# Kernel optimization log

Hardware: AMD Instinct MI355X
Metric: run time of the kernel (lower is better)

Reference implementation:

```python
import jax, jax.numpy as jnp
import numpy as np

EPS = 1e-5
B, N, K = 2, 20000, 17      # batch, num points, k+1 neighbors
CIN = 128                   # bn_size * growth_rate
G = 128                     # growth_rate


def index_points(pts, idx):
    # pts: [B, C, N], idx: [B, S, K] -> [B, C, S, K]
    return jnp.take_along_axis(pts[:, :, :, None], idx[:, None, :, :], axis=2)


def conv_bn_relu(x, W, b, gamma, beta, mean, var):
    # 1x1 Conv2d + BatchNorm2d (inference, running stats) + ReLU
    # x: [B, Cin, N, K], W: [Cout, Cin]
    y = jnp.einsum('oc,bcnk->bonk', W, x) + b[None, :, None, None]
    inv = gamma / jnp.sqrt(var + EPS)
    y = y * inv[None, :, None, None] + (beta - mean * inv)[None, :, None, None]
    return jax.nn.relu(y)


def setup_inputs() -> dict:
    key = jax.random.key(0)
    ks = jax.random.split(key, 16)
    feats = jax.random.normal(ks[0], (B, CIN, N), dtype=jnp.float32)
    pts = jax.random.normal(ks[1], (B, 3, N), dtype=jnp.float32)
    knn_idx = jax.random.randint(ks[2], (B, N, K), 0, N, dtype=jnp.int32)
    s = 0.05
    d = {
        'feats': feats, 'pts': pts, 'knn_idx': knn_idx,
        'Wd': jax.random.normal(ks[3], (G, 3), dtype=jnp.float32) * s,
        'bd': jnp.zeros((G,), jnp.float32),
        'gd': jnp.ones((G,), jnp.float32),
        'betad': jnp.zeros((G,), jnp.float32),
        'md': jax.random.normal(ks[4], (G,), dtype=jnp.float32) * 0.01,
        'vd': jax.random.uniform(ks[5], (G,), jnp.float32, 0.5, 1.5),
        'Wf': jax.random.normal(ks[6], (G, CIN), dtype=jnp.float32) * s,
        'bf': jnp.zeros((G,), jnp.float32),
        'gf': jnp.ones((G,), jnp.float32),
        'betaf': jnp.zeros((G,), jnp.float32),
        'mf': jax.random.normal(ks[7], (G,), dtype=jnp.float32) * 0.01,
        'vf': jax.random.uniform(ks[8], (G,), jnp.float32, 0.5, 1.5),
        'Wp': jax.random.normal(ks[9], (G, G), dtype=jnp.float32) * s,
        'bp': jnp.zeros((G,), jnp.float32),
        'gp': jnp.ones((G,), jnp.float32),
        'betap': jnp.zeros((G,), jnp.float32),
        'mp': jax.random.normal(ks[10], (G,), dtype=jnp.float32) * 0.01,
        'vp': jax.random.uniform(ks[11], (G,), jnp.float32, 0.5, 1.5),
    }
    return d


def reference(feats, pts, knn_idx,
              Wd, bd, gd, betad, md, vd,
              Wf, bf, gf, betaf, mf, vf,
              Wp, bp, gp, betap, mp, vp):
    # Point3DConv.forward with precomputed knn_idx
    knn_pts = index_points(pts, knn_idx)                 # [B,3,N,K]
    knn_delta = knn_pts - pts[:, :, :, None]             # [B,3,N,K]
    knn_delta = conv_bn_relu(knn_delta, Wd, bd, gd, betad, md, vd)   # [B,G,N,K]
    knn_feats = index_points(feats, knn_idx)              # [B,CIN,N,K]
    knn_feats = conv_bn_relu(knn_feats, Wf, bf, gf, betaf, mf, vf)   # [B,G,N,K]
    new_feats = knn_delta * knn_feats                     # [B,G,N,K]
    new_feats = conv_bn_relu(new_feats, Wp, bp, gp, betap, mp, vp)   # [B,G,N,K]
    return new_feats.sum(axis=-1)                         # [B,G,N]
```

## Files before the change

kernel.cpp:

```cpp
#include <hip/hip_runtime.h>
#include <hip/hip_bf16.h>
#include <cstdint>
#include <cstddef>

#define NB 2
#define NPT 20000
#define KNN 17
#define CH 128
#define NT16 (NPT/16)
#define NT32 (NPT/32)
#define EPSV 1e-5f

typedef short short8 __attribute__((ext_vector_type(8)));
typedef float f32x4 __attribute__((ext_vector_type(4)));
typedef float f32x2 __attribute__((ext_vector_type(2)));
typedef unsigned short u16;

__device__ __forceinline__ unsigned cvtpk(float lo, float hi) {
    unsigned r;
    asm("v_cvt_pk_bf16_f32 %0, %1, %2" : "=v"(r) : "v"(lo), "v"(hi));
    return r;
}
__device__ __forceinline__ u16 f2bf1(float x) {
    return (u16)cvtpk(x, x);
}
__device__ __forceinline__ f32x2 bfpair(unsigned w) {
    union { unsigned u; float f; } lo, hi;
    lo.u = w << 16; hi.u = w & 0xffff0000u;
    f32x2 r; r[0] = lo.f; r[1] = hi.f; return r;
}
__device__ __forceinline__ short8 packrow_scaled(const float* wrow, float s) {
    float4 w0 = *(const float4*)(wrow);
    float4 w1 = *(const float4*)(wrow + 4);
    uint4 uu;
    uu.x = cvtpk(w0.x*s, w0.y*s); uu.y = cvtpk(w0.z*s, w0.w*s);
    uu.z = cvtpk(w1.x*s, w1.y*s); uu.w = cvtpk(w1.z*s, w1.w*s);
    union { uint4 u; short8 s8; } cv; cv.u = uu; return cv.s8;
}
__device__ __forceinline__ short8 packrow(const float* wrow) {
    return packrow_scaled(wrow, 1.0f);
}
__device__ __forceinline__ void lds_barrier() {
    asm volatile("s_waitcnt lgkmcnt(0)\n\ts_barrier" ::: "memory");
}

__global__ __launch_bounds__(256) void k_feats(
    const float* __restrict__ feats, const float* __restrict__ Wf,
    const float* __restrict__ bfv, const float* __restrict__ gf,
    const float* __restrict__ betaf, const float* __restrict__ mf,
    const float* __restrict__ vf, u16* __restrict__ Fout)
{
    __shared__ u16 A_lds[32][136];
    __shared__ u16 O_lds[32][136];
    const int t  = threadIdx.x;
    const int b  = blockIdx.x / NT32;
    const int n0 = (blockIdx.x % NT32) * 32;

    {
        const int chunk = t & 7;
        const int cbase = t >> 3;
        const float* base = feats + (size_t)b*CH*NPT + n0 + chunk*4;
        #pragma unroll
        for (int it = 0; it < 4; ++it) {
            int c = it*32 + cbase;
            float4 v = *(const float4*)(base + (size_t)c*NPT);
            A_lds[chunk*4+0][c] = f2bf1(v.x);
            A_lds[chunk*4+1][c] = f2bf1(v.y);
            A_lds[chunk*4+2][c] = f2bf1(v.z);
            A_lds[chunk*4+3][c] = f2bf1(v.w);
        }
    }

    const int lane = t & 63, wid = t >> 6;
    const int h = lane >> 4, r16 = lane & 15;
    const int gb = wid * 32;

    short8 bfrag[2][4];
    float sf[2], tf[2];
    #pragma unroll
    for (int T = 0; T < 2; ++T) {
        int g = gb + T*16 + r16;
        #pragma unroll
        for (int s = 0; s < 4; ++s)
            bfrag[T][s] = packrow(Wf + g*CH + s*32 + h*8);
        float inv = gf[g] * rsqrtf(vf[g] + EPSV);
        sf[T] = inv;
        tf[T] = bfv[g]*inv + betaf[g] - mf[g]*inv;
    }
    lds_barrier();

    #pragma unroll
    for (int sub = 0; sub < 2; ++sub) {
        short8 a[4];
        #pragma unroll
        for (int s = 0; s < 4; ++s)
            a[s] = *(const short8*)&A_lds[sub*16 + r16][s*32 + h*8];
        #pragma unroll
        for (int T = 0; T < 2; ++T) {
            f32x4 acc = {0.f, 0.f, 0.f, 0.f};
            #pragma unroll
            for (int s = 0; s < 4; ++s)
                acc = __builtin_amdgcn_mfma_f32_16x16x32_bf16(a[s], bfrag[T][s], acc, 0, 0, 0);
            #pragma unroll
            for (int r = 0; r < 4; ++r) {
                float y = fmaxf(fmaf(sf[T], acc[r], tf[T]), 0.f);
                O_lds[sub*16 + 4*h + r][gb + T*16 + r16] = f2bf1(y);
            }
        }
    }
    lds_barrier();

    {
        const int pp = t >> 3, cc = (t & 7) * 16;
        uint4 v0 = *(const uint4*)&O_lds[pp][cc];
        uint4 v1 = *(const uint4*)&O_lds[pp][cc + 8];
        u16* dst = Fout + ((size_t)b*NPT + n0 + pp)*CH + cc;
        *(uint4*)dst = v0;
        *(uint4*)(dst + 8) = v1;
    }
}

struct Pref { float4 m; uint4 f; };

__global__ __launch_bounds__(256) void k_main(
    const float* __restrict__ pts, const int* __restrict__ knn,
    const u16* __restrict__ F,
    const float* __restrict__ Wd, const float* __restrict__ bd,
    const float* __restrict__ gd, const float* __restrict__ betad,
    const float* __restrict__ md, const float* __restrict__ vd,
    const float* __restrict__ Wp, const float* __restrict__ bp,
    const float* __restrict__ gp, const float* __restrict__ betap,
    const float* __restrict__ mp, const float* __restrict__ vp,
    float* __restrict__ out)
{
    __shared__ u16   Abuf[2][16*128];
    __shared__ float4 meta[16][KNN];

    const int t  = threadIdx.x;
    const int b  = blockIdx.x / NT16;
    const int n0 = (blockIdx.x % NT16) * 16;

    const float* px = pts + (size_t)b*3*NPT;
    const float* py = px + NPT;
    const float* pz = py + NPT;

    {
        const int* krow = knn + ((size_t)b*NPT + n0)*KNN;
        #pragma unroll 1
        for (int tau = t; tau < 16*KNN; tau += 256) {
            int r  = tau / KNN;
            int nb = krow[tau];
            float4 m;
            m.x = px[nb] - px[n0+r];
            m.y = py[nb] - py[n0+r];
            m.z = pz[nb] - pz[n0+r];
            m.w = __int_as_float(nb);
            (&meta[0][0])[tau] = m;
        }
    }
    lds_barrier();

    const int p_t = t >> 4, j_t = t & 15, c0 = j_t*8;
    const int lane = t & 63, wid = t >> 6;
    const int h = lane >> 4, r16 = lane & 15;
    const int gb = wid * 32;
    const u16* Fbj = F + (size_t)b*NPT*CH + c0;

    const int wOff = p_t*128 + (c0 ^ ((p_t&7)*8));
    int rOff[4];
    #pragma unroll
    for (int s = 0; s < 4; ++s)
        rOff[s] = r16*128 + ((s*32 + h*8) ^ ((r16&7)*8));

    auto issueK = [&](int k)->Pref {
        Pref P;
        P.m = meta[p_t][k];
        int nb = __float_as_int(P.m.w);
        P.f = *(const uint4*)(Fbj + (size_t)nb*CH);
        return P;
    };

    Pref PA = issueK(0);
    Pref PB = issueK(1);

    short8 bfrag[2][4];
    float tpv[2];
    #pragma unroll
    for (int T = 0; T < 2; ++T) {
        int g = gb + T*16 + r16;
        float inv = gp[g] * rsqrtf(vp[g] + EPSV);
        #pragma unroll
        for (int s = 0; s < 4; ++s)
            bfrag[T][s] = packrow_scaled(Wp + g*CH + s*32 + h*8, inv);
        tpv[T] = bp[g]*inv + betap[g] - mp[g]*inv;
    }

    f32x2 wx2[4], wy2[4], wz2[4], t2[4];
    #pragma unroll
    for (int q = 0; q < 4; ++q) {
        const int ca = c0 + 2*q, cb = ca + 1;
        float inva = gd[ca] * rsqrtf(vd[ca] + EPSV);
        float invb = gd[cb] * rsqrtf(vd[cb] + EPSV);
        wx2[q][0] = Wd[ca*3+0]*inva; wx2[q][1] = Wd[cb*3+0]*invb;
        wy2[q][0] = Wd[ca*3+1]*inva; wy2[q][1] = Wd[cb*3+1]*invb;
        wz2[q][0] = Wd[ca*3+2]*inva; wz2[q][1] = Wd[cb*3+2]*invb;
        t2[q][0]  = bd[ca]*inva + betad[ca] - md[ca]*inva;
        t2[q][1]  = bd[cb]*invb + betad[cb] - md[cb]*invb;
    }

    auto stage = [&](u16* A, const Pref& P) {
        const unsigned fw[4] = {P.f.x, P.f.y, P.f.z, P.f.w};
        const f32x2 z2 = {0.f, 0.f};
        unsigned pk[4];
        #pragma unroll
        for (int q = 0; q < 4; ++q) {
            f32x2 d = wx2[q]*P.m.x + wy2[q]*P.m.y + wz2[q]*P.m.z + t2[q];
            d = __builtin_elementwise_max(d, z2);
            f32x2 pr = d * bfpair(fw[q]);
            pk[q] = cvtpk(pr[0], pr[1]);
        }
        uint4 v; v.x = pk[0]; v.y = pk[1]; v.z = pk[2]; v.w = pk[3];
        *(uint4*)(A + wOff) = v;
    };

    f32x4 facc[2] = {};
    auto mfmaP = [&](const u16* A) {
        short8 a[4];
        #pragma unroll
        for (int s = 0; s < 4; ++s)
            a[s] = *(const short8*)(A + rOff[s]);
        #pragma unroll
        for (int T = 0; T < 2; ++T) {
            f32x4 acc = {0.f,0.f,0.f,0.f};
            #pragma unroll
            for (int s = 0; s < 4; ++s)
                acc = __builtin_amdgcn_mfma_f32_16x16x32_bf16(a[s], bfrag[T][s], acc, 0, 0, 0);
            f32x4 nt = {-tpv[T], -tpv[T], -tpv[T], -tpv[T]};
            facc[T] += __builtin_elementwise_max(acc, nt);
        }
    };

    stage(Abuf[0], PA);
    PA = PB;
    PB = issueK(2);
    lds_barrier();

    int p = 0;
    #pragma unroll 1
    for (int k = 0; k < 16; ++k) {
        stage(Abuf[p^1], PA);
        PA = PB;
        if (k + 3 <= 16) PB = issueK(k+3);
        mfmaP(Abuf[p]);
        lds_barrier();
        p ^= 1;
    }
    mfmaP(Abuf[p]);

    #pragma unroll
    for (int T = 0; T < 2; ++T) {
        int g = gb + T*16 + r16;
        f32x4 o = facc[T] + (float)KNN * tpv[T];
        *(f32x4*)(out + ((size_t)b*CH + g)*NPT + n0 + 4*h) = o;
    }
}

extern "C" void kernel_launch(void* const* d_in, const int* in_sizes, int n_in,
                              void* d_out, int out_size, void* d_ws, size_t ws_size,
                              hipStream_t stream)
{
    const float* feats = (const float*)d_in[0];
    const float* pts   = (const float*)d_in[1];
    const int*   knn   = (const int*)d_in[2];
    const float* Wd    = (const float*)d_in[3];
    const float* bd    = (const float*)d_in[4];
    const float* gd    = (const float*)d_in[5];
    const float* betad = (const float*)d_in[6];
    const float* md    = (const float*)d_in[7];
    const float* vd    = (const float*)d_in[8];
    const float* Wf    = (const float*)d_in[9];
    const float* bfv   = (const float*)d_in[10];
    const float* gf    = (const float*)d_in[11];
    const float* betaf = (const float*)d_in[12];
    const float* mf    = (const float*)d_in[13];
    const float* vf    = (const float*)d_in[14];
    const float* Wp    = (const float*)d_in[15];
    const float* bp    = (const float*)d_in[16];
    const float* gp    = (const float*)d_in[17];
    const float* betap = (const float*)d_in[18];
    const float* mp    = (const float*)d_in[19];
    const float* vp    = (const float*)d_in[20];
    float* out = (float*)d_out;
    u16* Fws = (u16*)d_ws;

    k_feats<<<dim3(NB * NT32), 256, 0, stream>>>(feats, Wf, bfv, gf, betaf, mf, vf, Fws);
    k_main <<<dim3(NB * NT16), 256, 0, stream>>>(pts, knn, Fws, Wd, bd, gd, betad, md, vd,
                                                 Wp, bp, gp, betap, mp, vp, out);
}
```

Measured before the change: 84.01 us.

## Process 32 points per block with 4-plane batched staging and deeper prefetch

The main kernel now handles two 16-point tiles per block, flattening the (tile, neighbor) pairs into 34 planes. Each loop iteration stages and prefetches four planes at a time into double-buffered LDS, which cuts barriers per plane and deepens the gather prefetch. The neighbor index is pre-shifted into a byte offset, and packed fp32 FMA/mul instructions are emitted explicitly. In exchange, the grid has half as many blocks, LDS and register use are larger, and the pipeline tail is hand-unrolled with more complex control.

```diff
diff --git a/kernel.cpp b/kernel.cpp
--- a/kernel.cpp
+++ b/kernel.cpp
@@ -7,8 +7,10 @@
 #define NPT 20000
 #define KNN 17
 #define CH 128
-#define NT16 (NPT/16)
 #define NT32 (NPT/32)
+#define NPB 32
+#define NTILE 2
+#define NPLANES (NTILE*KNN)
 #define EPSV 1e-5f
 
 typedef short short8 __attribute__((ext_vector_type(8)));
@@ -21,8 +23,16 @@
     asm("v_cvt_pk_bf16_f32 %0, %1, %2" : "=v"(r) : "v"(lo), "v"(hi));
     return r;
 }
-__device__ __forceinline__ u16 f2bf1(float x) {
-    return (u16)cvtpk(x, x);
+__device__ __forceinline__ u16 f2bf1(float x) { return (u16)cvtpk(x, x); }
+__device__ __forceinline__ f32x2 pk_fma(f32x2 a, f32x2 b, f32x2 c) {
+    f32x2 d;
+    asm("v_pk_fma_f32 %0, %1, %2, %3" : "=v"(d) : "v"(a), "v"(b), "v"(c));
+    return d;
+}
+__device__ __forceinline__ f32x2 pk_mul(f32x2 a, f32x2 b) {
+    f32x2 d;
+    asm("v_pk_mul_f32 %0, %1, %2" : "=v"(d) : "v"(a), "v"(b));
+    return d;
 }
 __device__ __forceinline__ f32x2 bfpair(unsigned w) {
     union { unsigned u; float f; } lo, hi;
@@ -133,29 +143,32 @@
     const float* __restrict__ mp, const float* __restrict__ vp,
     float* __restrict__ out)
 {
-    __shared__ u16   Abuf[2][16*128];
-    __shared__ float4 meta[16][KNN];
+    __shared__ u16   Abuf[2][4][16*128];
+    __shared__ float4 metaL[NPLANES][16];
 
     const int t  = threadIdx.x;
-    const int b  = blockIdx.x / NT16;
-    const int n0 = (blockIdx.x % NT16) * 16;
+    const int b  = blockIdx.x / NT32;
+    const int n0 = (blockIdx.x % NT32) * NPB;
 
     const float* px = pts + (size_t)b*3*NPT;
     const float* py = px + NPT;
     const float* pz = py + NPT;
 
     {
-        const int* krow = knn + ((size_t)b*NPT + n0)*KNN;
+        const int* kbase = knn + ((size_t)b*NPT + n0)*KNN;
         #pragma unroll 1
-        for (int tau = t; tau < 16*KNN; tau += 256) {
-            int r  = tau / KNN;
-            int nb = krow[tau];
+        for (int e = t; e < NPLANES*16; e += 256) {
+            int pi = e >> 4, p = e & 15;
+            int tile = (pi >= KNN) ? 1 : 0;
+            int k  = pi - tile*KNN;
+            int row = tile*16 + p;
+            int nb = kbase[row*KNN + k];
             float4 m;
-            m.x = px[nb] - px[n0+r];
-            m.y = py[nb] - py[n0+r];
-            m.z = pz[nb] - pz[n0+r];
-            m.w = __int_as_float(nb);
-            (&meta[0][0])[tau] = m;
+            m.x = px[nb] - px[n0+row];
+            m.y = py[nb] - py[n0+row];
+            m.z = pz[nb] - pz[n0+row];
+            m.w = __int_as_float(nb << 8);
+            metaL[pi][p] = m;
         }
     }
     lds_barrier();
@@ -164,7 +177,7 @@
     const int lane = t & 63, wid = t >> 6;
     const int h = lane >> 4, r16 = lane & 15;
     const int gb = wid * 32;
-    const u16* Fbj = F + (size_t)b*NPT*CH + c0;
+    const char* FbjB = (const char*)(F + (size_t)b*NPT*CH + c0);
 
     const int wOff = p_t*128 + (c0 ^ ((p_t&7)*8));
     int rOff[4];
@@ -172,16 +185,16 @@
     for (int s = 0; s < 4; ++s)
         rOff[s] = r16*128 + ((s*32 + h*8) ^ ((r16&7)*8));
 
-    auto issueK = [&](int k)->Pref {
+    auto issueK = [&](int pi)->Pref {
         Pref P;
-        P.m = meta[p_t][k];
-        int nb = __float_as_int(P.m.w);
-        P.f = *(const uint4*)(Fbj + (size_t)nb*CH);
+        P.m = metaL[pi][p_t];
+        P.f = *(const uint4*)(FbjB + __float_as_int(P.m.w));
         return P;
     };
 
-    Pref PA = issueK(0);
-    Pref PB = issueK(1);
+    Pref P[4];
+    #pragma unroll
+    for (int i = 0; i < 4; ++i) P[i] = issueK(i);
 
     short8 bfrag[2][4];
     float tpv[2];
@@ -208,27 +221,28 @@
         t2[q][1]  = bd[cb]*invb + betad[cb] - md[cb]*invb;
     }
 
-    auto stage = [&](u16* A, const Pref& P) {
-        const unsigned fw[4] = {P.f.x, P.f.y, P.f.z, P.f.w};
+    auto stage = [&](u16* plane, const Pref& Pr) {
+        const unsigned fw[4] = {Pr.f.x, Pr.f.y, Pr.f.z, Pr.f.w};
         const f32x2 z2 = {0.f, 0.f};
+        f32x2 dx2 = {Pr.m.x, Pr.m.x}, dy2 = {Pr.m.y, Pr.m.y}, dz2 = {Pr.m.z, Pr.m.z};
         unsigned pk[4];
         #pragma unroll
         for (int q = 0; q < 4; ++q) {
-            f32x2 d = wx2[q]*P.m.x + wy2[q]*P.m.y + wz2[q]*P.m.z + t2[q];
+            f32x2 d = pk_fma(wx2[q], dx2, pk_fma(wy2[q], dy2, pk_fma(wz2[q], dz2, t2[q])));
             d = __builtin_elementwise_max(d, z2);
-            f32x2 pr = d * bfpair(fw[q]);
+            f32x2 pr = pk_mul(d, bfpair(fw[q]));
             pk[q] = cvtpk(pr[0], pr[1]);
         }
         uint4 v; v.x = pk[0]; v.y = pk[1]; v.z = pk[2]; v.w = pk[3];
-        *(uint4*)(A + wOff) = v;
+        *(uint4*)(plane + wOff) = v;
     };
 
     f32x4 facc[2] = {};
-    auto mfmaP = [&](const u16* A) {
+    auto mfmaP = [&](const u16* plane) {
         short8 a[4];
         #pragma unroll
         for (int s = 0; s < 4; ++s)
-            a[s] = *(const short8*)(A + rOff[s]);
+            a[s] = *(const short8*)(plane + rOff[s]);
         #pragma unroll
         for (int T = 0; T < 2; ++T) {
             f32x4 acc = {0.f,0.f,0.f,0.f};
@@ -239,30 +253,57 @@
             facc[T] += __builtin_elementwise_max(acc, nt);
         }
     };
-
-    stage(Abuf[0], PA);
-    PA = PB;
-    PB = issueK(2);
+    auto writeout = [&](int tile) {
+        #pragma unroll
+        for (int T = 0; T < 2; ++T) {
+            int g = gb + T*16 + r16;
+            f32x4 o = facc[T] + (float)KNN * tpv[T];
+            *(f32x4*)(out + ((size_t)b*CH + g)*NPT + n0 + tile*16 + 4*h) = o;
+            facc[T][0]=0.f; facc[T][1]=0.f; facc[T][2]=0.f; facc[T][3]=0.f;
+        }
+    };
+
+    #pragma unroll
+    for (int i = 0; i < 4; ++i) stage(Abuf[0][i], P[i]);
+    #pragma unroll
+    for (int i = 0; i < 4; ++i) P[i] = issueK(4+i);
     lds_barrier();
 
-    int p = 0;
     #pragma unroll 1
-    for (int k = 0; k < 16; ++k) {
-        stage(Abuf[p^1], PA);
-        PA = PB;
-        if (k + 3 <= 16) PB = issueK(k+3);
-        mfmaP(Abuf[p]);
+    for (int c = 0; c < 6; ++c) {
+        const int H = c & 1;
+        u16* sb = &Abuf[H^1][0][0];
+        #pragma unroll
+        for (int i = 0; i < 4; ++i) stage(sb + i*2048, P[i]);
+        #pragma unroll
+        for (int i = 0; i < 4; ++i) P[i] = issueK(4*c + 8 + i);
+        const u16* mb = &Abuf[H][0][0];
+        #pragma unroll
+        for (int i = 0; i < 4; ++i) {
+            mfmaP(mb + i*2048);
+            if (i == 0 && c == 4) writeout(0);
+        }
         lds_barrier();
-        p ^= 1;
-    }
-    mfmaP(Abuf[p]);
-
-    #pragma unroll
-    for (int T = 0; T < 2; ++T) {
-        int g = gb + T*16 + r16;
-        f32x4 o = facc[T] + (float)KNN * tpv[T];
-        *(f32x4*)(out + ((size_t)b*CH + g)*NPT + n0 + 4*h) = o;
-    }
+    }
+    {
+        #pragma unroll
+        for (int i = 0; i < 4; ++i) stage(&Abuf[1][i][0], P[i]);
+        P[0] = issueK(32);
+        P[1] = issueK(33);
+        #pragma unroll
+        for (int i = 0; i < 4; ++i) mfmaP(&Abuf[0][i][0]);
+        lds_barrier();
+    }
+    {
+        stage(&Abuf[0][0][0], P[0]);
+        stage(&Abuf[0][1][0], P[1]);
+        #pragma unroll
+        for (int i = 0; i < 4; ++i) mfmaP(&Abuf[1][i][0]);
+        lds_barrier();
+    }
+    mfmaP(&Abuf[0][0][0]);
+    mfmaP(&Abuf[0][1][0]);
+    writeout(1);
 }
 
 extern "C" void kernel_launch(void* const* d_in, const int* in_sizes, int n_in,
@@ -294,6 +335,6 @@
     u16* Fws = (u16*)d_ws;
 
     k_feats<<<dim3(NB * NT32), 256, 0, stream>>>(feats, Wf, bfv, gf, betaf, mf, vf, Fws);
-    k_main <<<dim3(NB * NT16), 256, 0, stream>>>(pts, knn, Fws, Wd, bd, gd, betad, md, vd,
+    k_main <<<dim3(NB * NT32), 256, 0, stream>>>(pts, knn, Fws, Wd, bd, gd, betad, md, vd,
                                                  Wp, bp, gp, betap, mp, vp, out);
 }
```

New measurement: 75.54 us. 10.1% less time.

## Process neighbor pairs per barrier with deeper prefetch and packed FMA staging

Applied to the files above, without the earlier changes.

Restructures the K-loop so each LDS barrier covers two neighbor slices instead of one. The double buffer now holds two planes per stage, and four neighbor prefetches are kept in flight, which halves the number of barriers and deepens the latency hiding for the gathered feature loads. The meta table is transposed to [K][16], and neighbor indices are pre-shifted to byte offsets so the gather address needs no multiply. The delta conv math is written with explicit v_pk_fma/v_pk_mul. The cost is more registers per thread and a fully hand-unrolled schedule.

```diff
diff --git a/kernel.cpp b/kernel.cpp
--- a/kernel.cpp
+++ b/kernel.cpp
@@ -21,8 +21,16 @@
     asm("v_cvt_pk_bf16_f32 %0, %1, %2" : "=v"(r) : "v"(lo), "v"(hi));
     return r;
 }
-__device__ __forceinline__ u16 f2bf1(float x) {
-    return (u16)cvtpk(x, x);
+__device__ __forceinline__ u16 f2bf1(float x) { return (u16)cvtpk(x, x); }
+__device__ __forceinline__ f32x2 pk_fma(f32x2 a, f32x2 b, f32x2 c) {
+    f32x2 d;
+    asm("v_pk_fma_f32 %0, %1, %2, %3" : "=v"(d) : "v"(a), "v"(b), "v"(c));
+    return d;
+}
+__device__ __forceinline__ f32x2 pk_mul(f32x2 a, f32x2 b) {
+    f32x2 d;
+    asm("v_pk_mul_f32 %0, %1, %2" : "=v"(d) : "v"(a), "v"(b));
+    return d;
 }
 __device__ __forceinline__ f32x2 bfpair(unsigned w) {
     union { unsigned u; float f; } lo, hi;
@@ -133,8 +141,8 @@
     const float* __restrict__ mp, const float* __restrict__ vp,
     float* __restrict__ out)
 {
-    __shared__ u16   Abuf[2][16*128];
-    __shared__ float4 meta[16][KNN];
+    __shared__ u16    Abuf[2][2][16*128];
+    __shared__ float4 metaL[KNN][16];
 
     const int t  = threadIdx.x;
     const int b  = blockIdx.x / NT16;
@@ -147,15 +155,15 @@
     {
         const int* krow = knn + ((size_t)b*NPT + n0)*KNN;
         #pragma unroll 1
-        for (int tau = t; tau < 16*KNN; tau += 256) {
-            int r  = tau / KNN;
-            int nb = krow[tau];
+        for (int e = t; e < KNN*16; e += 256) {
+            int k = e >> 4, p = e & 15;
+            int nb = krow[p*KNN + k];
             float4 m;
-            m.x = px[nb] - px[n0+r];
-            m.y = py[nb] - py[n0+r];
-            m.z = pz[nb] - pz[n0+r];
-            m.w = __int_as_float(nb);
-            (&meta[0][0])[tau] = m;
+            m.x = px[nb] - px[n0+p];
+            m.y = py[nb] - py[n0+p];
+            m.z = pz[nb] - pz[n0+p];
+            m.w = __int_as_float(nb << 8);
+            metaL[k][p] = m;
         }
     }
     lds_barrier();
@@ -164,7 +172,7 @@
     const int lane = t & 63, wid = t >> 6;
     const int h = lane >> 4, r16 = lane & 15;
     const int gb = wid * 32;
-    const u16* Fbj = F + (size_t)b*NPT*CH + c0;
+    const char* FbjB = (const char*)(F + (size_t)b*NPT*CH + c0);
 
     const int wOff = p_t*128 + (c0 ^ ((p_t&7)*8));
     int rOff[4];
@@ -174,14 +182,13 @@
 
     auto issueK = [&](int k)->Pref {
         Pref P;
-        P.m = meta[p_t][k];
-        int nb = __float_as_int(P.m.w);
-        P.f = *(const uint4*)(Fbj + (size_t)nb*CH);
+        P.m = metaL[k][p_t];
+        P.f = *(const uint4*)(FbjB + __float_as_int(P.m.w));
         return P;
     };
 
-    Pref PA = issueK(0);
-    Pref PB = issueK(1);
+    Pref PA0 = issueK(0), PA1 = issueK(1);
+    Pref PB0 = issueK(2), PB1 = issueK(3);
 
     short8 bfrag[2][4];
     float tpv[2];
@@ -208,27 +215,28 @@
         t2[q][1]  = bd[cb]*invb + betad[cb] - md[cb]*invb;
     }
 
-    auto stage = [&](u16* A, const Pref& P) {
-        const unsigned fw[4] = {P.f.x, P.f.y, P.f.z, P.f.w};
+    auto stage = [&](u16* plane, const Pref& Pr) {
+        const unsigned fw[4] = {Pr.f.x, Pr.f.y, Pr.f.z, Pr.f.w};
         const f32x2 z2 = {0.f, 0.f};
+        f32x2 dx2 = {Pr.m.x, Pr.m.x}, dy2 = {Pr.m.y, Pr.m.y}, dz2 = {Pr.m.z, Pr.m.z};
         unsigned pk[4];
         #pragma unroll
         for (int q = 0; q < 4; ++q) {
-            f32x2 d = wx2[q]*P.m.x + wy2[q]*P.m.y + wz2[q]*P.m.z + t2[q];
+            f32x2 d = pk_fma(wx2[q], dx2, pk_fma(wy2[q], dy2, pk_fma(wz2[q], dz2, t2[q])));
             d = __builtin_elementwise_max(d, z2);
-            f32x2 pr = d * bfpair(fw[q]);
+            f32x2 pr = pk_mul(d, bfpair(fw[q]));
             pk[q] = cvtpk(pr[0], pr[1]);
         }
         uint4 v; v.x = pk[0]; v.y = pk[1]; v.z = pk[2]; v.w = pk[3];
-        *(uint4*)(A + wOff) = v;
+        *(uint4*)(plane + wOff) = v;
     };
 
     f32x4 facc[2] = {};
-    auto mfmaP = [&](const u16* A) {
+    auto mfmaP = [&](const u16* plane) {
         short8 a[4];
         #pragma unroll
         for (int s = 0; s < 4; ++s)
-            a[s] = *(const short8*)(A + rOff[s]);
+            a[s] = *(const short8*)(plane + rOff[s]);
         #pragma unroll
         for (int T = 0; T < 2; ++T) {
             f32x4 acc = {0.f,0.f,0.f,0.f};
@@ -240,22 +248,37 @@
         }
     };
 
-    stage(Abuf[0], PA);
-    PA = PB;
-    PB = issueK(2);
-    lds_barrier();
-
-    int p = 0;
-    #pragma unroll 1
-    for (int k = 0; k < 16; ++k) {
-        stage(Abuf[p^1], PA);
-        PA = PB;
-        if (k + 3 <= 16) PB = issueK(k+3);
-        mfmaP(Abuf[p]);
+    u16* B0 = &Abuf[0][0][0];
+    u16* B1 = &Abuf[1][0][0];
+
+    auto chunk = [&](u16* sb, const u16* mb, Pref& S0, Pref& S1, int r0, int r1) {
+        stage(sb, S0);
+        stage(sb + 2048, S1);
+        if (r0 >= 0) S0 = issueK(r0);
+        if (r1 >= 0) S1 = issueK(r1);
+        mfmaP(mb);
+        mfmaP(mb + 2048);
         lds_barrier();
-        p ^= 1;
-    }
-    mfmaP(Abuf[p]);
+    };
+
+    stage(B0, PA0);
+    stage(B0 + 2048, PA1);
+    PA0 = issueK(4); PA1 = issueK(5);
+    lds_barrier();
+
+    chunk(B1, B0, PB0, PB1,  6,  7);
+    chunk(B0, B1, PA0, PA1,  8,  9);
+    chunk(B1, B0, PB0, PB1, 10, 11);
+    chunk(B0, B1, PA0, PA1, 12, 13);
+    chunk(B1, B0, PB0, PB1, 14, 15);
+    chunk(B0, B1, PA0, PA1, 16, -1);
+    chunk(B1, B0, PB0, PB1, -1, -1);
+
+    stage(B0, PA0);
+    mfmaP(B1);
+    mfmaP(B1 + 2048);
+    lds_barrier();
+    mfmaP(B0);
 
     #pragma unroll
     for (int T = 0; T < 2; ++T) {
```

Result: no change. 82.45 us (-1.9%).
